# Kernel optimization log

Hardware: AMD Instinct MI355X
Metric: run time of the kernel (lower is better)

## Reference

```python
import jax, jax.numpy as jnp
import numpy as np

EPS_AGG = 1e-6  # torch code adds 1e-6 to scatter weight sums
EPS_BN = 1e-5


def _pix_idx(loc_orig, H, W):
    # map normalized coords in [-1,1] to flat pixel index on an HxW grid
    loc = jnp.clip(loc_orig, -1.0, 1.0) * 0.5 + 0.5
    ix = jnp.round(loc[..., 0] * (W - 1)).astype(jnp.int32)
    iy = jnp.round(loc[..., 1] * (H - 1)).astype(jnp.int32)
    return iy * W + ix  # [B, N0]


def token2map(x, loc_orig, idx_agg, H, W):
    # scatter token features to a dense map, averaging collisions
    B, N, C = x.shape
    N0 = idx_agg.shape[1]
    idx_hw = _pix_idx(loc_orig, H, W)                                   # [B, N0]
    tok = jnp.take_along_axis(x, idx_agg[..., None], axis=1)            # [B, N0, C]
    flat = (idx_hw + jnp.arange(B, dtype=jnp.int32)[:, None] * (H * W)).reshape(-1)
    sums = jax.ops.segment_sum(tok.reshape(-1, C), flat, num_segments=B * H * W)
    cnt = jax.ops.segment_sum(jnp.ones((B * N0,), x.dtype), flat, num_segments=B * H * W)
    out = sums / (cnt[:, None] + EPS_AGG)
    return out.reshape(B, H, W, C).transpose(0, 3, 1, 2)                # [B, C, H, W]


def map2token(fmap, Nt, loc_orig, idx_agg_t, agg_weight_t):
    # gather map pixels back to Nt target tokens, weighted-averaging per token
    B, C, H, W = fmap.shape
    idx_hw = _pix_idx(loc_orig, H, W)                                   # [B, N0]
    pix = fmap.transpose(0, 2, 3, 1).reshape(B, H * W, C)
    gath = jnp.take_along_axis(pix, idx_hw[..., None], axis=1)          # [B, N0, C]
    flat = (idx_agg_t + jnp.arange(B, dtype=jnp.int32)[:, None] * Nt).reshape(-1)
    num = jax.ops.segment_sum((gath * agg_weight_t[..., None]).reshape(-1, C), flat, num_segments=B * Nt)
    den = jax.ops.segment_sum(agg_weight_t.reshape(-1), flat, num_segments=B * Nt)
    return (num / (den[:, None] + EPS_AGG)).reshape(B, Nt, C)


def token_downup(x, idx_agg_s, idx_agg_t, agg_weight_t, Nt):
    # weighted aggregation from N source tokens to Nt target tokens via N0 original positions
    B, N, C = x.shape
    src = jnp.take_along_axis(x, idx_agg_s[..., None], axis=1)          # [B, N0, C]
    flat = (idx_agg_t + jnp.arange(B, dtype=jnp.int32)[:, None] * Nt).reshape(-1)
    num = jax.ops.segment_sum((src * agg_weight_t[..., None]).reshape(-1, C), flat, num_segments=B * Nt)
    den = jax.ops.segment_sum(agg_weight_t.reshape(-1), flat, num_segments=B * Nt)
    return (num / (den[:, None] + EPS_AGG)).reshape(B, Nt, C)


def batchnorm(x, gamma, beta):
    # BatchNorm2d on [B,C,Nt,1] == per-channel stats over (B, Nt); x here is [B, Nt, C]
    mu = x.mean(axis=(0, 1), keepdims=True)
    var = x.var(axis=(0, 1), keepdims=True)
    return (x - mu) * jax.lax.rsqrt(var + EPS_BN) * gamma + beta


def setup_inputs() -> dict:
    key = jax.random.key(0)
    ks = jax.random.split(key, 12)
    B, N, N0, Nt, Cin, Cout, H, W = 32, 1568, 3136, 784, 256, 512, 56, 56
    x = jax.random.normal(ks[0], (B, N, Cin), dtype=jnp.float32)
    loc_orig = jax.random.uniform(ks[1], (B, N0, 2), dtype=jnp.float32, minval=-1.0, maxval=1.0)
    idx_agg = jax.random.randint(ks[2], (B, N0), 0, N, dtype=jnp.int32)
    agg_weight = jax.random.uniform(ks[3], (B, N0), dtype=jnp.float32)
    idx_agg_t = jax.random.randint(ks[4], (B, N0), 0, Nt, dtype=jnp.int32)
    agg_weight_t = jax.random.uniform(ks[5], (B, N0), dtype=jnp.float32)
    dw_w = jax.random.normal(ks[6], (Cin, 1, 3, 3), dtype=jnp.float32) * 0.1     # depthwise 3x3
    skip_w = jax.random.normal(ks[7], (Cin,), dtype=jnp.float32) * 0.1           # depthwise 1x1
    conv_w = jax.random.normal(ks[8], (Cout, Cin), dtype=jnp.float32) * (1.0 / np.sqrt(Cin))
    gamma1 = jnp.ones((Cin,), jnp.float32); beta1 = jnp.zeros((Cin,), jnp.float32)
    gamma2 = jnp.ones((Cout,), jnp.float32); beta2 = jnp.zeros((Cout,), jnp.float32)
    return {"x": x, "loc_orig": loc_orig, "idx_agg": idx_agg, "agg_weight": agg_weight,
            "idx_agg_t": idx_agg_t, "agg_weight_t": agg_weight_t, "H": H, "W": W, "Nt": Nt,
            "dw_w": dw_w, "skip_w": skip_w, "conv_w": conv_w,
            "gamma1": gamma1, "beta1": beta1, "gamma2": gamma2, "beta2": beta2}


def reference(x, loc_orig, idx_agg, agg_weight, idx_agg_t, agg_weight_t, H, W, Nt,
              dw_w, skip_w, conv_w, gamma1, beta1, gamma2, beta2):
    # token -> map scatter
    x_map = token2map(x, loc_orig, idx_agg, H, W)                       # [B, Cin, H, W]
    # 3x3 depthwise conv, stride 2, padding 1
    Cin = x_map.shape[1]
    x_map = jax.lax.conv_general_dilated(
        x_map, dw_w, window_strides=(2, 2), padding=((1, 1), (1, 1)),
        feature_group_count=Cin, dimension_numbers=("NCHW", "OIHW", "NCHW"))    # [B, Cin, H/2, W/2]
    # map -> target tokens gather
    x_back = map2token(x_map, Nt, loc_orig, idx_agg_t, agg_weight_t)    # [B, Nt, Cin]
    # skip path: token downsample + 1x1 depthwise (per-channel scale)
    xs = token_downup(x, idx_agg, idx_agg_t, agg_weight_t, Nt)          # [B, Nt, Cin]
    xs = xs * skip_w                                                    # dw_skip, groups=Cin, k=1
    y = xs + x_back
    y = batchnorm(y, gamma1, beta1)
    y = jnp.einsum("bnc,oc->bno", y, conv_w)                            # 1x1 conv Cin->Cout
    y = batchnorm(y, gamma2, beta2)
    return jax.nn.relu(y)                                               # [B, Nt, Cout]
```

## Files before the change

kernel.cpp:

```cpp
#include <hip/hip_runtime.h>

constexpr int B    = 32;
constexpr int N    = 1568;
constexpr int N0   = 3136;
constexpr int Nt   = 784;
constexpr int Cin  = 256;
constexpr int Cout = 512;
constexpr int H    = 56;
constexpr int W    = 56;
constexpr int HW   = 3136;
constexpr int Ho   = 28;
constexpr int Wo   = 28;
constexpr int HWo  = 784;
constexpr int RR   = B * Nt;
constexpr int NE   = B * N0;
constexpr int NBP  = B * HW;
constexpr int NBT  = B * Nt;
constexpr int NB   = NBP + NBT;
constexpr int NCHUNK = NB / 256;

constexpr size_t W_HIST  = 0;
constexpr size_t W_S1SUM = NB;
constexpr size_t W_S1SQ  = W_S1SUM + Cin;
constexpr size_t W_S2SUM = W_S1SQ + Cin;
constexpr size_t W_S2SQ  = W_S2SUM + Cout;
constexpr size_t W_OFF   = NB + 1536;
constexpr size_t W_CUR   = W_OFF + NB + 8;
constexpr size_t W_P56   = W_CUR + NB;
constexpr size_t W_P28   = W_P56 + NE;
constexpr size_t W_BSUM  = W_P28 + NE;
constexpr size_t W_SRTS  = W_BSUM + 512;
constexpr size_t W_STS   = W_SRTS + NE;
constexpr size_t W_STP   = W_STS + NE;
constexpr size_t W_STW   = W_STP + NE;
constexpr size_t W_CONVB = W_STW + NE;
constexpr size_t W_YBF   = W_CONVB + (size_t)B * HWo * Cin / 2;
constexpr size_t W_WFB   = W_YBF + (size_t)RR * Cin / 2;
constexpr size_t W_BIAS  = W_WFB + (size_t)Cout * Cin / 2;
constexpr size_t W_A2    = W_BIAS + Cout;
constexpr size_t W_C2    = W_A2 + Cout;
constexpr size_t W_ZB    = W_C2 + Cout;

__device__ __forceinline__ int pix_of(float t, float scale) {
    t = fminf(fmaxf(t, -1.0f), 1.0f);
    float u = __fadd_rn(__fmul_rn(t, 0.5f), 0.5f);
    return (int)rintf(__fmul_rn(u, scale));
}
__device__ __forceinline__ unsigned short f2bf(float f) {
    unsigned int u = __float_as_uint(f);
    u = (u + 0x7fffu + ((u >> 16) & 1u)) >> 16;
    return (unsigned short)u;
}
__device__ __forceinline__ float bf2f(unsigned short h) {
    return __uint_as_float(((unsigned int)h) << 16);
}

__global__ void k_hist(const float* __restrict__ loc, const int* __restrict__ idxt,
                       int* __restrict__ hist, int* __restrict__ p56a, int* __restrict__ p28a) {
    int i = blockIdx.x * 256 + threadIdx.x;
    if (i >= NE) return;
    int b = i / N0;
    float lx = loc[(size_t)2 * i], ly = loc[(size_t)2 * i + 1];
    int p56 = pix_of(ly, 55.0f) * W + pix_of(lx, 55.0f);
    int p28 = pix_of(ly, 27.0f) * Wo + pix_of(lx, 27.0f);
    p56a[i] = p56; p28a[i] = p28;
    atomicAdd(&hist[b * HW + p56], 1);
    atomicAdd(&hist[NBP + b * Nt + idxt[i]], 1);
}

__global__ void k_scanA(const int* __restrict__ hist, int* __restrict__ bsum) {
    __shared__ int sm[256];
    int i = blockIdx.x * 256 + threadIdx.x;
    sm[threadIdx.x] = hist[i];
    __syncthreads();
    for (int d = 128; d > 0; d >>= 1) {
        if (threadIdx.x < d) sm[threadIdx.x] += sm[threadIdx.x + d];
        __syncthreads();
    }
    if (threadIdx.x == 0) bsum[blockIdx.x] = sm[0];
}

__global__ void k_scanB(int* __restrict__ bsum) {
    __shared__ int sm[512];
    int t = threadIdx.x;
    int v = (t < NCHUNK) ? bsum[t] : 0;
    sm[t] = v; __syncthreads();
    for (int d = 1; d < 512; d <<= 1) {
        int u = (t >= d) ? sm[t - d] : 0;
        __syncthreads();
        sm[t] += u;
        __syncthreads();
    }
    if (t < NCHUNK) bsum[t] = sm[t] - v;
}

__global__ void k_scanC(const int* __restrict__ hist, const int* __restrict__ bsum,
                        int* __restrict__ off, int* __restrict__ cur) {
    __shared__ int sm[256];
    int t = threadIdx.x;
    int i = blockIdx.x * 256 + t;
    int v = hist[i];
    sm[t] = v; __syncthreads();
    for (int d = 1; d < 256; d <<= 1) {
        int u = (t >= d) ? sm[t - d] : 0;
        __syncthreads();
        sm[t] += u;
        __syncthreads();
    }
    int excl = bsum[blockIdx.x] + sm[t] - v;
    off[i] = excl; cur[i] = excl;
    if (i == NB - 1) off[NB] = excl + v;
}

__global__ void k_scatteridx(const int* __restrict__ p56a, const int* __restrict__ p28a,
                             const int* __restrict__ idxa, const int* __restrict__ idxt,
                             const float* __restrict__ wt, int* __restrict__ cur,
                             int* __restrict__ srtS, int* __restrict__ sTs,
                             int* __restrict__ sTp, float* __restrict__ sTw) {
    int i = blockIdx.x * 256 + threadIdx.x;
    if (i >= NE) return;
    int b = i / N0;
    int s = idxa[i];
    int posP = atomicAdd(&cur[b * HW + p56a[i]], 1);
    srtS[posP] = s;
    int posT = atomicAdd(&cur[NBP + b * Nt + idxt[i]], 1) - NE;
    sTs[posT] = s; sTp[posT] = p28a[i]; sTw[posT] = wt[i];
}

constexpr int GCAP = 512;
__global__ __launch_bounds__(256) void k_gconv(const float* __restrict__ x,
        const int* __restrict__ off, const int* __restrict__ srtS,
        const float* __restrict__ dww, unsigned short* __restrict__ convb) {
    __shared__ int   sPk[GCAP];
    __shared__ float sRc[GCAP];
    __shared__ int sSt[9], sCt[9], sPref[10];
    int blk = blockIdx.x;
    int c   = threadIdx.x;
    int b   = blk / HWo;
    int rem = blk - b * HWo;
    int oy  = rem / Wo;
    int ox  = rem - oy * Wo;
    if (c < 9) {
        int ky = c / 3, kx = c - ky * 3;
        int iy = oy * 2 - 1 + ky, ix = ox * 2 - 1 + kx;
        int st = 0, ct = 0;
        if (iy >= 0 && iy < H && ix >= 0 && ix < W) {
            int bin = b * HW + iy * W + ix;
            st = off[bin];
            ct = off[bin + 1] - st;
        }
        sSt[c] = st; sCt[c] = ct;
    }
    __syncthreads();
    if (c == 0) {
        int a = 0;
#pragma unroll
        for (int k = 0; k < 9; ++k) { sPref[k] = a; a += sCt[k]; }
        sPref[9] = a;
    }
    __syncthreads();
    int T = sPref[9];
    float wv[9];
#pragma unroll
    for (int k = 0; k < 9; ++k) wv[k] = dww[c * 9 + k];
    float acc = 0.0f;
    for (int base = 0; base < T; base += GCAP) {
        if (c < 9) {
            int ct = sCt[c], pr = sPref[c], st = sSt[c];
            float rc = 1.0f / ((float)ct + 1e-6f);
            int j0 = max(base - pr, 0);
            int j1 = min(base + GCAP - pr, ct);
            for (int j = j0; j < j1; ++j) {
                sPk[pr + j - base] = srtS[st + j] | (c << 16);
                sRc[pr + j - base] = rc;
            }
        }
        __syncthreads();
        int cnt = min(T - base, GCAP);
        for (int j = 0; j < cnt; ++j) {
            int pk = sPk[j];
            float rc = sRc[j];
            int s = pk & 0xFFFF, tap = pk >> 16;
            acc = fmaf(x[((size_t)b * N + s) * Cin + c] * rc, wv[tap], acc);
        }
        __syncthreads();
    }
    convb[(size_t)blk * Cin + c] = f2bf(acc);
}

constexpr int TCAP = 256;
__global__ __launch_bounds__(256) void k_gtok(const float* __restrict__ x,
        const unsigned short* __restrict__ convb, const int* __restrict__ off,
        const int* __restrict__ sTs, const int* __restrict__ sTp,
        const float* __restrict__ sTw, const float* __restrict__ skipw,
        unsigned short* __restrict__ ybf) {
    __shared__ int sS[TCAP];
    __shared__ int sP[TCAP];
    __shared__ float sW[TCAP];
    int bt = blockIdx.x;
    int c  = threadIdx.x;
    int b  = bt / Nt;
    int st = off[NBP + bt] - NE, en = off[NBP + bt + 1] - NE;
    int T = en - st;
    float sk = skipw[c];
    float acc = 0.0f, wsum = 0.0f;
    for (int base = 0; base < T; base += TCAP) {
        int cnt = min(T - base, TCAP);
        if (c < cnt) {
            sS[c] = sTs[st + base + c];
            sP[c] = sTp[st + base + c];
            sW[c] = sTw[st + base + c];
        }
        __syncthreads();
        for (int j = 0; j < cnt; ++j) {
            int s = sS[j], p = sP[j];
            float w = sW[j];
            wsum += w;
            float cv = bf2f(convb[((size_t)b * HWo + p) * Cin + c]);
            acc = fmaf(w, cv + sk * x[((size_t)b * N + s) * Cin + c], acc);
        }
        __syncthreads();
    }
    ybf[(size_t)bt * Cin + c] = f2bf(acc * (1.0f / (wsum + 1e-6f)));
}

__global__ void k_ystats(const unsigned short* __restrict__ ybf,
                         float* __restrict__ s1, float* __restrict__ s1q) {
    int c = threadIdx.x;
    float sum = 0.0f, sq = 0.0f;
    for (int r = blockIdx.x; r < RR; r += gridDim.x) {
        float v = bf2f(ybf[(size_t)r * Cin + c]);
        sum += v;
        sq = fmaf(v, v, sq);
    }
    atomicAdd(&s1[c], sum);
    atomicAdd(&s1q[c], sq);
}

__global__ void k_fold(const float* __restrict__ s1, const float* __restrict__ s1q,
                       const float* __restrict__ g1, const float* __restrict__ b1,
                       const float* __restrict__ convw, unsigned short* __restrict__ wfb,
                       float* __restrict__ bias) {
    int o = blockIdx.x, c = threadIdx.x;
    const float inv = 1.0f / (float)RR;
    float mu  = s1[c] * inv;
    float var = s1q[c] * inv - mu * mu;
    float a   = g1[c] / sqrtf(var + 1e-5f);
    float bs  = b1[c] - mu * a;
    float wv  = convw[(size_t)o * Cin + c];
    wfb[(size_t)o * Cin + c] = f2bf(wv * a);
    __shared__ float red[256];
    red[c] = wv * bs;
    __syncthreads();
    for (int st = 128; st > 0; st >>= 1) {
        if (c < st) red[c] += red[c + st];
        __syncthreads();
    }
    if (c == 0) bias[o] = red[0];
}

typedef __attribute__((ext_vector_type(8))) short short8;
typedef __attribute__((ext_vector_type(4))) float f32x4;

__global__ __launch_bounds__(256) void k_gemm(const unsigned short* __restrict__ A,
        const unsigned short* __restrict__ Bt, const float* __restrict__ bias,
        unsigned short* __restrict__ zb, float* __restrict__ s2, float* __restrict__ s2q) {
    constexpr int BK = 32, LS = 48;
    __shared__ unsigned short As[128 * LS];
    __shared__ unsigned short Bs[128 * LS];
    __shared__ float rsum[128], rsq[128];
    int m0 = blockIdx.x * 128, n0 = blockIdx.y * 128;
    int t = threadIdx.x;
    int wave = t >> 6, lane = t & 63;
    int wm = wave >> 1, wn = wave & 1;
    int l16 = lane & 15, lq = lane >> 4;
    f32x4 acc[4][4];
#pragma unroll
    for (int i = 0; i < 4; ++i)
#pragma unroll
        for (int j = 0; j < 4; ++j) acc[i][j] = (f32x4)0.0f;
    if (t < 128) { rsum[t] = 0.0f; rsq[t] = 0.0f; }

    for (int k0 = 0; k0 < Cin; k0 += BK) {
#pragma unroll
        for (int r2 = 0; r2 < 2; ++r2) {
            int e = r2 * 256 + t;
            int row = e >> 2, kc = (e & 3) * 8;
            *(float4*)&As[row * LS + kc] = *(const float4*)&A[((size_t)(m0 + row)) * Cin + k0 + kc];
            *(float4*)&Bs[row * LS + kc] = *(const float4*)&Bt[((size_t)(n0 + row)) * Cin + k0 + kc];
        }
        __syncthreads();
        short8 af[4], bf[4];
#pragma unroll
        for (int i = 0; i < 4; ++i) {
            af[i] = *(short8*)&As[(wm * 64 + i * 16 + l16) * LS + lq * 8];
            bf[i] = *(short8*)&Bs[(wn * 64 + i * 16 + l16) * LS + lq * 8];
        }
#pragma unroll
        for (int i = 0; i < 4; ++i)
#pragma unroll
            for (int j = 0; j < 4; ++j)
                acc[i][j] = __builtin_amdgcn_mfma_f32_16x16x32_bf16(af[i], bf[j], acc[i][j], 0, 0, 0);
        __syncthreads();
    }
#pragma unroll
    for (int j = 0; j < 4; ++j) {
        int cl  = wn * 64 + j * 16 + l16;
        int col = n0 + cl;
        float bv = bias[col];
        float ps = 0.0f, pq = 0.0f;
#pragma unroll
        for (int i = 0; i < 4; ++i) {
            int rbase = m0 + wm * 64 + i * 16 + lq * 4;
#pragma unroll
            for (int r = 0; r < 4; ++r) {
                float v = acc[i][j][r] + bv;
                zb[(size_t)(rbase + r) * Cout + col] = f2bf(v);
                ps += v;
                pq = fmaf(v, v, pq);
            }
        }
        atomicAdd(&rsum[cl], ps);
        atomicAdd(&rsq[cl], pq);
    }
    __syncthreads();
    if (t < 128) {
        atomicAdd(&s2[n0 + t], rsum[t]);
        atomicAdd(&s2q[n0 + t], rsq[t]);
    }
}

__global__ void k_fold2(const float* __restrict__ s2, const float* __restrict__ s2q,
                        const float* __restrict__ g2, const float* __restrict__ b2,
                        float* __restrict__ a2, float* __restrict__ c2) {
    int o = threadIdx.x;
    const float inv = 1.0f / (float)RR;
    float mu  = s2[o] * inv;
    float var = s2q[o] * inv - mu * mu;
    float a   = g2[o] / sqrtf(var + 1e-5f);
    a2[o] = a;
    c2[o] = b2[o] - mu * a;
}

__global__ void k_final(const unsigned short* __restrict__ zb, const float* __restrict__ a2,
                        const float* __restrict__ c2, float* __restrict__ out) {
    size_t j4 = ((size_t)blockIdx.x * 256 + threadIdx.x) * 4;
    int o = (int)(j4 & (Cout - 1));
    uint2 u = *(const uint2*)&zb[j4];
    float e0 = bf2f((unsigned short)(u.x & 0xffffu));
    float e1 = bf2f((unsigned short)(u.x >> 16));
    float e2 = bf2f((unsigned short)(u.y & 0xffffu));
    float e3 = bf2f((unsigned short)(u.y >> 16));
    float4 r;
    r.x = fmaxf(fmaf(e0, a2[o + 0], c2[o + 0]), 0.0f);
    r.y = fmaxf(fmaf(e1, a2[o + 1], c2[o + 1]), 0.0f);
    r.z = fmaxf(fmaf(e2, a2[o + 2], c2[o + 2]), 0.0f);
    r.w = fmaxf(fmaf(e3, a2[o + 3], c2[o + 3]), 0.0f);
    *(float4*)&out[j4] = r;
}

extern "C" void kernel_launch(void* const* d_in, const int* in_sizes, int n_in,
                              void* d_out, int out_size, void* d_ws, size_t ws_size,
                              hipStream_t stream) {
    const float* x     = (const float*)d_in[0];
    const float* loc   = (const float*)d_in[1];
    const int*   idxa  = (const int*)d_in[2];
    const int*   idxt  = (const int*)d_in[4];
    const float* wt    = (const float*)d_in[5];
    const float* dww   = (const float*)d_in[9];
    const float* skipw = (const float*)d_in[10];
    const float* convw = (const float*)d_in[11];
    const float* g1    = (const float*)d_in[12];
    const float* b1    = (const float*)d_in[13];
    const float* g2    = (const float*)d_in[14];
    const float* b2    = (const float*)d_in[15];

    float* ws = (float*)d_ws;
    int*   hist  = (int*)(ws + W_HIST);
    float* s1sum = ws + W_S1SUM;
    float* s1sq  = ws + W_S1SQ;
    float* s2sum = ws + W_S2SUM;
    float* s2sq  = ws + W_S2SQ;
    int*   off   = (int*)(ws + W_OFF);
    int*   cur   = (int*)(ws + W_CUR);
    int*   p56a  = (int*)(ws + W_P56);
    int*   p28a  = (int*)(ws + W_P28);
    int*   bsum  = (int*)(ws + W_BSUM);
    int*   srtS  = (int*)(ws + W_SRTS);
    int*   sTs   = (int*)(ws + W_STS);
    int*   sTp   = (int*)(ws + W_STP);
    float* sTw   = ws + W_STW;
    unsigned short* convb = (unsigned short*)(ws + W_CONVB);
    unsigned short* ybf   = (unsigned short*)(ws + W_YBF);
    unsigned short* wfb   = (unsigned short*)(ws + W_WFB);
    float* bias  = ws + W_BIAS;
    float* a2    = ws + W_A2;
    float* c2    = ws + W_C2;
    unsigned short* zb = (unsigned short*)(ws + W_ZB);
    float* out   = (float*)d_out;

    hipMemsetAsync(hist, 0, (size_t)(NB + 1536) * sizeof(float), stream);

    k_hist<<<NE / 256, 256, 0, stream>>>(loc, idxt, hist, p56a, p28a);
    k_scanA<<<NCHUNK, 256, 0, stream>>>(hist, bsum);
    k_scanB<<<1, 512, 0, stream>>>(bsum);
    k_scanC<<<NCHUNK, 256, 0, stream>>>(hist, bsum, off, cur);
    k_scatteridx<<<NE / 256, 256, 0, stream>>>(p56a, p28a, idxa, idxt, wt, cur, srtS, sTs, sTp, sTw);

    k_gconv<<<B * HWo, 256, 0, stream>>>(x, off, srtS, dww, convb);
    k_gtok<<<NBT, 256, 0, stream>>>(x, convb, off, sTs, sTp, sTw, skipw, ybf);
    k_ystats<<<256, 256, 0, stream>>>(ybf, s1sum, s1sq);
    k_fold<<<Cout, 256, 0, stream>>>(s1sum, s1sq, g1, b1, convw, wfb, bias);

    dim3 gg(RR / 128, Cout / 128);
    k_gemm<<<gg, 256, 0, stream>>>(ybf, wfb, bias, zb, s2sum, s2sq);
    k_fold2<<<1, 512, 0, stream>>>(s2sum, s2sq, g2, b2, a2, c2);
    k_final<<<(int)(((size_t)RR * Cout) / 1024), 256, 0, stream>>>(zb, a2, c2, out);
}
```

Measured before the change: 303.1 us.

## Pre-cast token features to bf16 and unroll gather loops with multiple accumulators

Adds a kernel that converts x to bf16 once, so the conv-gather and token-gather kernels read half the bytes per random gather. The gather loops are unrolled by 4 and 2 with independent accumulators to keep more loads in flight. Depthwise weights are moved into shared memory instead of a register array indexed by tap. In exchange there is an extra pass over x, an added rounding of inputs to bf16, and roughly 9 KB more shared memory per block.

After: 314.0 us. +3.6%, slower.

```diff
diff --git a/kernel.cpp b/kernel.cpp
--- a/kernel.cpp
+++ b/kernel.cpp
@@ -18,6 +18,7 @@
 constexpr int NBT  = B * Nt;
 constexpr int NB   = NBP + NBT;
 constexpr int NCHUNK = NB / 256;
+constexpr size_t XTOT = (size_t)B * N * Cin;
 
 constexpr size_t W_HIST  = 0;
 constexpr size_t W_S1SUM = NB;
@@ -40,6 +41,7 @@
 constexpr size_t W_A2    = W_BIAS + Cout;
 constexpr size_t W_C2    = W_A2 + Cout;
 constexpr size_t W_ZB    = W_C2 + Cout;
+constexpr size_t W_XH    = W_ZB + (size_t)RR * Cout / 2;
 
 __device__ __forceinline__ int pix_of(float t, float scale) {
     t = fminf(fmaxf(t, -1.0f), 1.0f);
@@ -53,6 +55,15 @@
 }
 __device__ __forceinline__ float bf2f(unsigned short h) {
     return __uint_as_float(((unsigned int)h) << 16);
+}
+
+__global__ void k_cast(const float* __restrict__ x, uint2* __restrict__ xh2) {
+    size_t i = (size_t)blockIdx.x * 256 + threadIdx.x;
+    float4 v = *(const float4*)&x[i * 4];
+    uint2 o;
+    o.x = (unsigned int)f2bf(v.x) | ((unsigned int)f2bf(v.y) << 16);
+    o.y = (unsigned int)f2bf(v.z) | ((unsigned int)f2bf(v.w) << 16);
+    xh2[i] = o;
 }
 
 __global__ void k_hist(const float* __restrict__ loc, const int* __restrict__ idxt,
@@ -128,11 +139,12 @@
 }
 
 constexpr int GCAP = 512;
-__global__ __launch_bounds__(256) void k_gconv(const float* __restrict__ x,
+__global__ __launch_bounds__(256) void k_gconv(const unsigned short* __restrict__ xh,
         const int* __restrict__ off, const int* __restrict__ srtS,
         const float* __restrict__ dww, unsigned short* __restrict__ convb) {
     __shared__ int   sPk[GCAP];
     __shared__ float sRc[GCAP];
+    __shared__ float sWv[9 * 256];
     __shared__ int sSt[9], sCt[9], sPref[10];
     int blk = blockIdx.x;
     int c   = threadIdx.x;
@@ -140,6 +152,8 @@
     int rem = blk - b * HWo;
     int oy  = rem / Wo;
     int ox  = rem - oy * Wo;
+#pragma unroll
+    for (int k = 0; k < 9; ++k) sWv[k * 256 + c] = dww[c * 9 + k];
     if (c < 9) {
         int ky = c / 3, kx = c - ky * 3;
         int iy = oy * 2 - 1 + ky, ix = ox * 2 - 1 + kx;
@@ -160,10 +174,8 @@
     }
     __syncthreads();
     int T = sPref[9];
-    float wv[9];
-#pragma unroll
-    for (int k = 0; k < 9; ++k) wv[k] = dww[c * 9 + k];
-    float acc = 0.0f;
+    const unsigned short* xb = xh + (size_t)b * N * Cin + c;
+    float a0 = 0.0f, a1 = 0.0f, a2 = 0.0f, a3 = 0.0f;
     for (int base = 0; base < T; base += GCAP) {
         if (c < 9) {
             int ct = sCt[c], pr = sPref[c], st = sSt[c];
@@ -177,19 +189,31 @@
         }
         __syncthreads();
         int cnt = min(T - base, GCAP);
-        for (int j = 0; j < cnt; ++j) {
+        int j = 0;
+        for (; j + 4 <= cnt; j += 4) {
+            int pk0 = sPk[j], pk1 = sPk[j + 1], pk2 = sPk[j + 2], pk3 = sPk[j + 3];
+            float r0 = sRc[j], r1 = sRc[j + 1], r2 = sRc[j + 2], r3 = sRc[j + 3];
+            float x0 = bf2f(xb[(size_t)(pk0 & 0xFFFF) * Cin]);
+            float x1 = bf2f(xb[(size_t)(pk1 & 0xFFFF) * Cin]);
+            float x2 = bf2f(xb[(size_t)(pk2 & 0xFFFF) * Cin]);
+            float x3 = bf2f(xb[(size_t)(pk3 & 0xFFFF) * Cin]);
+            a0 = fmaf(x0 * r0, sWv[(pk0 >> 16) * 256 + c], a0);
+            a1 = fmaf(x1 * r1, sWv[(pk1 >> 16) * 256 + c], a1);
+            a2 = fmaf(x2 * r2, sWv[(pk2 >> 16) * 256 + c], a2);
+            a3 = fmaf(x3 * r3, sWv[(pk3 >> 16) * 256 + c], a3);
+        }
+        for (; j < cnt; ++j) {
             int pk = sPk[j];
-            float rc = sRc[j];
-            int s = pk & 0xFFFF, tap = pk >> 16;
-            acc = fmaf(x[((size_t)b * N + s) * Cin + c] * rc, wv[tap], acc);
-        }
-        __syncthreads();
-    }
-    convb[(size_t)blk * Cin + c] = f2bf(acc);
+            a0 = fmaf(bf2f(xb[(size_t)(pk & 0xFFFF) * Cin]) * sRc[j],
+                      sWv[(pk >> 16) * 256 + c], a0);
+        }
+        __syncthreads();
+    }
+    convb[(size_t)blk * Cin + c] = f2bf((a0 + a1) + (a2 + a3));
 }
 
 constexpr int TCAP = 256;
-__global__ __launch_bounds__(256) void k_gtok(const float* __restrict__ x,
+__global__ __launch_bounds__(256) void k_gtok(const unsigned short* __restrict__ xh,
         const unsigned short* __restrict__ convb, const int* __restrict__ off,
         const int* __restrict__ sTs, const int* __restrict__ sTp,
         const float* __restrict__ sTw, const float* __restrict__ skipw,
@@ -203,7 +227,9 @@
     int st = off[NBP + bt] - NE, en = off[NBP + bt + 1] - NE;
     int T = en - st;
     float sk = skipw[c];
-    float acc = 0.0f, wsum = 0.0f;
+    const unsigned short* xb = xh + (size_t)b * N * Cin + c;
+    const unsigned short* cb = convb + (size_t)b * HWo * Cin + c;
+    float acc0 = 0.0f, acc1 = 0.0f, wsum = 0.0f;
     for (int base = 0; base < T; base += TCAP) {
         int cnt = min(T - base, TCAP);
         if (c < cnt) {
@@ -212,16 +238,27 @@
             sW[c] = sTw[st + base + c];
         }
         __syncthreads();
-        for (int j = 0; j < cnt; ++j) {
-            int s = sS[j], p = sP[j];
-            float w = sW[j];
-            wsum += w;
-            float cv = bf2f(convb[((size_t)b * HWo + p) * Cin + c]);
-            acc = fmaf(w, cv + sk * x[((size_t)b * N + s) * Cin + c], acc);
-        }
-        __syncthreads();
-    }
-    ybf[(size_t)bt * Cin + c] = f2bf(acc * (1.0f / (wsum + 1e-6f)));
+        int j = 0;
+        for (; j + 2 <= cnt; j += 2) {
+            int s0 = sS[j], p0 = sP[j], s1 = sS[j + 1], p1 = sP[j + 1];
+            float w0 = sW[j], w1 = sW[j + 1];
+            float cv0 = bf2f(cb[(size_t)p0 * Cin]);
+            float xv0 = bf2f(xb[(size_t)s0 * Cin]);
+            float cv1 = bf2f(cb[(size_t)p1 * Cin]);
+            float xv1 = bf2f(xb[(size_t)s1 * Cin]);
+            wsum += w0 + w1;
+            acc0 = fmaf(w0, fmaf(sk, xv0, cv0), acc0);
+            acc1 = fmaf(w1, fmaf(sk, xv1, cv1), acc1);
+        }
+        if (j < cnt) {
+            int s0 = sS[j], p0 = sP[j];
+            float w0 = sW[j];
+            wsum += w0;
+            acc0 = fmaf(w0, fmaf(sk, bf2f(xb[(size_t)s0 * Cin]), bf2f(cb[(size_t)p0 * Cin])), acc0);
+        }
+        __syncthreads();
+    }
+    ybf[(size_t)bt * Cin + c] = f2bf((acc0 + acc1) * (1.0f / (wsum + 1e-6f)));
 }
 
 __global__ void k_ystats(const unsigned short* __restrict__ ybf,
@@ -397,18 +434,20 @@
     float* a2    = ws + W_A2;
     float* c2    = ws + W_C2;
     unsigned short* zb = (unsigned short*)(ws + W_ZB);
+    unsigned short* xh = (unsigned short*)(ws + W_XH);
     float* out   = (float*)d_out;
 
     hipMemsetAsync(hist, 0, (size_t)(NB + 1536) * sizeof(float), stream);
 
+    k_cast<<<(int)(XTOT / 4 / 256), 256, 0, stream>>>(x, (uint2*)xh);
     k_hist<<<NE / 256, 256, 0, stream>>>(loc, idxt, hist, p56a, p28a);
     k_scanA<<<NCHUNK, 256, 0, stream>>>(hist, bsum);
     k_scanB<<<1, 512, 0, stream>>>(bsum);
     k_scanC<<<NCHUNK, 256, 0, stream>>>(hist, bsum, off, cur);
     k_scatteridx<<<NE / 256, 256, 0, stream>>>(p56a, p28a, idxa, idxt, wt, cur, srtS, sTs, sTp, sTw);
 
-    k_gconv<<<B * HWo, 256, 0, stream>>>(x, off, srtS, dww, convb);
-    k_gtok<<<NBT, 256, 0, stream>>>(x, convb, off, sTs, sTp, sTw, skipw, ybf);
+    k_gconv<<<B * HWo, 256, 0, stream>>>(xh, off, srtS, dww, convb);
+    k_gtok<<<NBT, 256, 0, stream>>>(xh, convb, off, sTs, sTp, sTw, skipw, ybf);
     k_ystats<<<256, 256, 0, stream>>>(ybf, s1sum, s1sq);
     k_fold<<<Cout, 256, 0, stream>>>(s1sum, s1sq, g1, b1, convw, wfb, bias);
 
```
